# Kernel optimization log

Hardware: AMD Instinct MI355X
Metric: run time of the kernel (lower is better)

The kernel has to match this reference:

```python
import jax, jax.numpy as jnp
import numpy as np

N, C, H, W = 4, 256, 64, 64  # in_channels == out_channels == C


def conv1x1(x, w, b):
    # x: [N, Cin, H, W], w: [Cout, Cin], b: [Cout]
    return jnp.einsum('nchw,oc->nohw', x, w) + b[None, :, None, None]


def setup_inputs() -> dict:
    key = jax.random.key(0)
    ks = jax.random.split(key, 4)
    scale = 1.0 / np.sqrt(C)
    return {
        'x': jax.random.normal(ks[0], (N, C, H, W), dtype=jnp.float32),
        'theta_w': jax.random.normal(ks[1], (C, C), dtype=jnp.float32) * scale,
        'theta_b': jnp.zeros((C,), dtype=jnp.float32),
        'phi_w': jax.random.normal(ks[2], (C, C), dtype=jnp.float32) * scale,
        'phi_b': jnp.zeros((C,), dtype=jnp.float32),
        'conv1_w': jax.random.normal(ks[3], (C, C), dtype=jnp.float32) * scale,
        'conv1_b': jnp.zeros((C,), dtype=jnp.float32),
    }


def reference(x, theta_w, theta_b, phi_w, phi_b, conv1_w, conv1_b):
    n, c, h, w = x.shape
    hw = h * w
    theta = conv1x1(x, theta_w, theta_b).reshape(n, c, hw)   # queries [N,C,HW]
    phi = conv1x1(x, phi_w, phi_b).reshape(n, c, hw)         # keys    [N,C,HW]
    g = x.reshape(n, c, hw)                                   # values  [N,C,HW]
    # f = einsum('niab,nicd->nabcd') flattened: [N, HW_q, HW_k]
    scores = jnp.einsum('ncp,ncq->npq', theta, phi) / jnp.sqrt(jnp.asarray(c, x.dtype))
    attn = jax.nn.softmax(scores, axis=-1)                    # softmax over keys
    # f = einsum('nabcd,nicd->niab'): weighted sum of values
    f = jnp.einsum('npq,ncq->ncp', attn, g).reshape(n, c, h, w)
    result = conv1x1(f, conv1_w, conv1_b)
    return x + result
```

## Files before the change

kernel.cpp:

```cpp
#include <hip/hip_runtime.h>
#include <hip/hip_bf16.h>

typedef __attribute__((ext_vector_type(8))) short short8;
typedef __attribute__((ext_vector_type(4))) short short4_t;
typedef __attribute__((ext_vector_type(4))) float float4_t;
typedef unsigned short ushort;

#define HW 4096
#define CC 256
#define NBATCH 4
#define SEQ ((size_t)NBATCH * HW)

static __device__ __forceinline__ unsigned short f2b(float f) {
    union { float f; unsigned u; } v; v.f = f;
    unsigned r = v.u + 0x7FFF + ((v.u >> 16) & 1);
    return (unsigned short)(r >> 16);
}
static __device__ __forceinline__ float b2f(unsigned short u) {
    union { unsigned u; float f; } v; v.u = ((unsigned)u) << 16;
    return v.f;
}

__global__ __launch_bounds__(256) void k_prep(const float* __restrict__ x,
                                              const float* __restrict__ tw,
                                              const float* __restrict__ pw,
                                              const float* __restrict__ cw,
                                              unsigned short* __restrict__ XT,
                                              unsigned short* __restrict__ gb,
                                              unsigned short* __restrict__ Wbt,
                                              unsigned short* __restrict__ Wbp,
                                              unsigned short* __restrict__ Wbc) {
    __shared__ float T[64][65];
    int fb = blockIdx.x + 64 * (blockIdx.y + 4 * blockIdx.z);
    if (fb < 768) {
        int i = fb * 256 + threadIdx.x;
        int sel = i >> 16, off = i & 65535;
        const float* s = sel == 0 ? tw : (sel == 1 ? pw : cw);
        unsigned short* d = sel == 0 ? Wbt : (sel == 1 ? Wbp : Wbc);
        d[off] = f2b(s[off]);
    }
    int n = blockIdx.z, c0 = blockIdx.y * 64, p0 = blockIdx.x * 64;
    int t = threadIdx.x;
    int pl = t & 63, rg = t >> 6;
    const float* xp = x + ((size_t)n * CC + c0) * HW + p0;
    #pragma unroll
    for (int i = 0; i < 16; i++) {
        int cl = rg * 16 + i;
        float v = xp[(size_t)cl * HW + pl];
        T[cl][pl] = v;
        gb[((size_t)n * CC + c0 + cl) * HW + p0 + pl] = f2b(v);
    }
    __syncthreads();
    int cl = t & 63, pg = t >> 6;
    unsigned short* xt = XT + ((size_t)n * HW + p0) * CC + c0;
    #pragma unroll
    for (int i = 0; i < 16; i++) {
        int plw = pg * 16 + i;
        xt[(size_t)plw * CC + cl] = f2b(T[cl][plw]);
    }
}

__global__ __launch_bounds__(256) void k_proj(const unsigned short* __restrict__ XT,
                                              const unsigned short* __restrict__ Wt,
                                              const unsigned short* __restrict__ Wp,
                                              const float* __restrict__ bt,
                                              const float* __restrict__ bp,
                                              unsigned short* __restrict__ outT_t,
                                              unsigned short* __restrict__ outT_p) {
    const unsigned short* W; const float* b; unsigned short* outT;
    if (blockIdx.y == 0) { W = Wt; b = bt; outT = outT_t; }
    else                 { W = Wp; b = bp; outT = outT_p; }
    int w = threadIdx.x >> 6, lane = threadIdx.x & 63;
    int nidx = lane & 15, quad = lane >> 4;
    size_t row0 = (size_t)blockIdx.x * 64 + w * 16;
    float4_t acc[16];
    #pragma unroll
    for (int i = 0; i < 16; i++) acc[i] = (float4_t)(0.f);
    const unsigned short* arow = XT + (row0 + nidx) * CC + quad * 8;
    for (int ks = 0; ks < 8; ks++) {
        short8 a = *(const short8*)(arow + ks * 32);
        #pragma unroll
        for (int cb = 0; cb < 16; cb++) {
            short8 bb = *(const short8*)(W + (size_t)(cb * 16 + nidx) * CC + ks * 32 + quad * 8);
            acc[cb] = __builtin_amdgcn_mfma_f32_16x16x32_bf16(a, bb, acc[cb], 0, 0, 0);
        }
    }
    #pragma unroll
    for (int cb = 0; cb < 16; cb++) {
        int co = cb * 16 + nidx;
        float bias = b[co];
        #pragma unroll
        for (int r = 0; r < 4; r++) {
            size_t prow = row0 + quad * 4 + r;
            outT[prow * CC + co] = f2b(acc[cb][r] + bias);
        }
    }
}

__global__ __launch_bounds__(512)
void k_attn(const unsigned short* __restrict__ thetaT,
            const unsigned short* __restrict__ phiT,
            const unsigned short* __restrict__ gb,
            ushort* __restrict__ Ow, float* __restrict__ lw) {
    __shared__ __align__(16) ushort Kl[2][16384];
    __shared__ __align__(16) ushort Pbuf[2][16][64][8];
    __shared__ float Lbuf[2][128];

    const int tid = threadIdx.x;
    const int w = tid >> 6, lane = tid & 63;
    const int nidx = lane & 15, quad = lane >> 4;
    const int qg = w & 3;
    const int kh = w >> 2;
    const int nb = (blockIdx.x & 7) >> 1;
    const int h  = blockIdx.x & 1;
    const int qtile = blockIdx.x >> 3;
    const int p0 = qtile * 128;
    const size_t seq0 = (size_t)nb * HW;
    const ushort* Kg = phiT + seq0 * CC;
    const ushort* Vg = gb + (size_t)nb * CC * HW;
    const int k00 = h * 2048;

    short8 th[2][8];
    #pragma unroll
    for (int qs = 0; qs < 2; qs++) {
        const ushort* qrow = thetaT + (seq0 + p0 + qg * 32 + qs * 16 + nidx) * CC + quad * 8;
        #pragma unroll
        for (int kb = 0; kb < 8; kb++) th[qs][kb] = *(const short8*)(qrow + kb * 32);
    }

    float4_t o[2][8];
    #pragma unroll
    for (int i = 0; i < 2; i++)
        #pragma unroll
        for (int j = 0; j < 8; j++) o[i][j] = (float4_t)(0.f);
    float lrow[8];
    #pragma unroll
    for (int i = 0; i < 8; i++) lrow[i] = 0.f;

    const int c_s = tid >> 4, n_s = tid & 15;
    const int kfbase = (c_s >> 2) * 512 + ((c_s & 3) * 16 + n_s) * 8;
    auto loadKregs = [&](short8 (&kr)[4], int tt) {
        #pragma unroll
        for (int rr = 0; rr < 4; rr++)
            kr[rr] = *(const short8*)(Kg + (size_t)(k00 + tt * 64 + rr * 16 + n_s) * CC + c_s * 8);
    };
    auto stageK = [&](int buf, const short8 (&kr)[4]) {
        #pragma unroll
        for (int rr = 0; rr < 4; rr++) *(short8*)(&Kl[buf][rr * 4096 + kfbase]) = kr[rr];
    };
    auto loadVregs = [&](short8 (&vr)[4], int tt) {
        #pragma unroll
        for (int mg = 0; mg < 2; mg++)
            #pragma unroll
            for (int kst = 0; kst < 2; kst++)
                vr[mg * 2 + kst] = *(const short8*)(Vg + (size_t)(w * 32 + mg * 16 + nidx) * HW
                                                    + k00 + tt * 64 + kst * 32 + quad * 8);
    };

    const float SC = 0.0625f * 1.44269504088896f;
    const int pj = nidx & 7;
    const int pc_hi = nidx >> 3;

    float4_t s00, s01, s10, s11;
    auto expPhase = [&](int buf) {
        #pragma unroll
        for (int r = 0; r < 4; r++) {
            float e = exp2f(s00[r] * SC); lrow[r] += e;
            Pbuf[buf][(qg * 2 + 0) * 2 + kh][(0 * 2 + pc_hi) * 16 + quad * 4 + r][pj] = f2b(e);
        }
        #pragma unroll
        for (int r = 0; r < 4; r++) {
            float e = exp2f(s01[r] * SC); lrow[r] += e;
            Pbuf[buf][(qg * 2 + 0) * 2 + kh][(1 * 2 + pc_hi) * 16 + quad * 4 + r][pj] = f2b(e);
        }
        #pragma unroll
        for (int r = 0; r < 4; r++) {
            float e = exp2f(s10[r] * SC); lrow[4 + r] += e;
            Pbuf[buf][(qg * 2 + 1) * 2 + kh][(0 * 2 + pc_hi) * 16 + quad * 4 + r][pj] = f2b(e);
        }
        #pragma unroll
        for (int r = 0; r < 4; r++) {
            float e = exp2f(s11[r] * SC); lrow[4 + r] += e;
            Pbuf[buf][(qg * 2 + 1) * 2 + kh][(1 * 2 + pc_hi) * 16 + quad * 4 + r][pj] = f2b(e);
        }
    };

    short8 kregs[4], vregs[4];
    loadKregs(kregs, 0); loadVregs(vregs, 0);
    stageK(0, kregs);
    loadKregs(kregs, 1);
    __syncthreads();
    s00 = (float4_t)(0.f); s01 = (float4_t)(0.f); s10 = (float4_t)(0.f); s11 = (float4_t)(0.f);
    #pragma unroll
    for (int kb = 0; kb < 8; kb++) {
        short8 k0 = *(const short8*)(&Kl[0][((kh * 2 + 0) * 8 + kb) * 512 + lane * 8]);
        short8 k1 = *(const short8*)(&Kl[0][((kh * 2 + 1) * 8 + kb) * 512 + lane * 8]);
        s00 = __builtin_amdgcn_mfma_f32_16x16x32_bf16(th[0][kb], k0, s00, 0, 0, 0);
        s01 = __builtin_amdgcn_mfma_f32_16x16x32_bf16(th[0][kb], k1, s01, 0, 0, 0);
        s10 = __builtin_amdgcn_mfma_f32_16x16x32_bf16(th[1][kb], k0, s10, 0, 0, 0);
        s11 = __builtin_amdgcn_mfma_f32_16x16x32_bf16(th[1][kb], k1, s11, 0, 0, 0);
    }
    expPhase(0);
    stageK(1, kregs);
    loadKregs(kregs, 2);
    __syncthreads();

    #pragma unroll 1
    for (int t = 0; t < 31; t++) {
        const int pb = t & 1;
        const int kbuf = (t + 1) & 1;
        s00 = (float4_t)(0.f); s01 = (float4_t)(0.f);
        s10 = (float4_t)(0.f); s11 = (float4_t)(0.f);
        #pragma unroll
        for (int i = 0; i < 8; i++) {
            short8 k0 = *(const short8*)(&Kl[kbuf][((kh * 2 + 0) * 8 + i) * 512 + lane * 8]);
            short8 k1 = *(const short8*)(&Kl[kbuf][((kh * 2 + 1) * 8 + i) * 512 + lane * 8]);
            s00 = __builtin_amdgcn_mfma_f32_16x16x32_bf16(th[0][i], k0, s00, 0, 0, 0);
            s01 = __builtin_amdgcn_mfma_f32_16x16x32_bf16(th[0][i], k1, s01, 0, 0, 0);
            s10 = __builtin_amdgcn_mfma_f32_16x16x32_bf16(th[1][i], k0, s10, 0, 0, 0);
            s11 = __builtin_amdgcn_mfma_f32_16x16x32_bf16(th[1][i], k1, s11, 0, 0, 0);
            short8 pf0 = *(const short8*)(&Pbuf[pb][i * 2 + 0][lane][0]);
            short8 pf1 = *(const short8*)(&Pbuf[pb][i * 2 + 1][lane][0]);
            o[0][i] = __builtin_amdgcn_mfma_f32_16x16x32_bf16(vregs[0], pf0, o[0][i], 0, 0, 0);
            o[0][i] = __builtin_amdgcn_mfma_f32_16x16x32_bf16(vregs[1], pf1, o[0][i], 0, 0, 0);
            o[1][i] = __builtin_amdgcn_mfma_f32_16x16x32_bf16(vregs[2], pf0, o[1][i], 0, 0, 0);
            o[1][i] = __builtin_amdgcn_mfma_f32_16x16x32_bf16(vregs[3], pf1, o[1][i], 0, 0, 0);
        }
        loadVregs(vregs, t + 1);
        expPhase((t + 1) & 1);
        if (t < 30) {
            stageK((t + 2) & 1, kregs);
            loadKregs(kregs, (t + 3 < 32) ? t + 3 : 31);
        }
        __syncthreads();
    }
    {
        const int pb = 31 & 1;
        #pragma unroll
        for (int i = 0; i < 8; i++) {
            short8 pf0 = *(const short8*)(&Pbuf[pb][i * 2 + 0][lane][0]);
            short8 pf1 = *(const short8*)(&Pbuf[pb][i * 2 + 1][lane][0]);
            o[0][i] = __builtin_amdgcn_mfma_f32_16x16x32_bf16(vregs[0], pf0, o[0][i], 0, 0, 0);
            o[0][i] = __builtin_amdgcn_mfma_f32_16x16x32_bf16(vregs[1], pf1, o[0][i], 0, 0, 0);
            o[1][i] = __builtin_amdgcn_mfma_f32_16x16x32_bf16(vregs[2], pf0, o[1][i], 0, 0, 0);
            o[1][i] = __builtin_amdgcn_mfma_f32_16x16x32_bf16(vregs[3], pf1, o[1][i], 0, 0, 0);
        }
    }

    #pragma unroll
    for (int i = 0; i < 8; i++) {
        float v = lrow[i];
        v += __shfl_xor(v, 1);
        v += __shfl_xor(v, 2);
        v += __shfl_xor(v, 4);
        v += __shfl_xor(v, 8);
        if (nidx == 0)
            Lbuf[kh][qg * 32 + (i >> 2) * 16 + quad * 4 + (i & 3)] = v;
    }
    __syncthreads();
    if (tid < 128)
        lw[(size_t)h * SEQ + seq0 + p0 + tid] = Lbuf[0][tid] + Lbuf[1][tid];
    ushort* Op = Ow + ((size_t)h * SEQ + seq0 + p0) * CC;
    #pragma unroll
    for (int mg = 0; mg < 2; mg++)
        #pragma unroll
        for (int qq = 0; qq < 8; qq++) {
            short4_t pk;
            #pragma unroll
            for (int r = 0; r < 4; r++) pk[r] = (short)f2b(o[mg][qq][r]);
            *(short4_t*)(Op + (size_t)(qq * 16 + nidx) * CC + w * 32 + mg * 16 + quad * 4) = pk;
        }
}

__global__ __launch_bounds__(256) void k_reduce(const ushort* __restrict__ Ow,
                                                const float* __restrict__ lw,
                                                unsigned short* __restrict__ fT) {
    const short8* O0 = (const short8*)Ow;
    const short8* O1 = (const short8*)(Ow + SEQ * CC);
    int i0 = blockIdx.x * 256 + threadIdx.x;
    #pragma unroll
    for (int j = 0; j < 4; j++) {
        int idx = j * 131072 + i0;
        int row = idx >> 5;
        float li = 1.0f / (lw[row] + lw[SEQ + row]);
        short8 a = O0[idx];
        short8 b = O1[idx];
        short8 pk;
        #pragma unroll
        for (int r = 0; r < 8; r++)
            pk[r] = (short)f2b((b2f((ushort)a[r]) + b2f((ushort)b[r])) * li);
        *(short8*)(fT + (size_t)idx * 8) = pk;
    }
}

__global__ __launch_bounds__(256) void k_final(const unsigned short* __restrict__ Wc,
                                               const float* __restrict__ bc,
                                               const unsigned short* __restrict__ fT,
                                               const float* __restrict__ x,
                                               float* __restrict__ out) {
    int w = threadIdx.x >> 6, lane = threadIdx.x & 63;
    int nidx = lane & 15, quad = lane >> 4;
    int n = blockIdx.z;
    int co0 = blockIdx.y * 64 + w * 16;
    int p0 = blockIdx.x * 64;
    float4_t acc[4];
    #pragma unroll
    for (int i = 0; i < 4; i++) acc[i] = (float4_t)(0.f);
    const unsigned short* arow = Wc + (size_t)(co0 + nidx) * CC + quad * 8;
    const unsigned short* brow = fT + ((size_t)n * HW + p0 + nidx) * CC + quad * 8;
    for (int ks = 0; ks < 8; ks++) {
        short8 a = *(const short8*)(arow + ks * 32);
        #pragma unroll
        for (int pb = 0; pb < 4; pb++) {
            short8 bb = *(const short8*)(brow + (size_t)pb * 16 * CC + ks * 32);
            acc[pb] = __builtin_amdgcn_mfma_f32_16x16x32_bf16(a, bb, acc[pb], 0, 0, 0);
        }
    }
    #pragma unroll
    for (int pb = 0; pb < 4; pb++) {
        #pragma unroll
        for (int r = 0; r < 4; r++) {
            int co = co0 + quad * 4 + r;
            size_t idx = ((size_t)n * CC + co) * HW + p0 + pb * 16 + nidx;
            out[idx] = x[idx] + bc[co] + acc[pb][r];
        }
    }
}

extern "C" void kernel_launch(void* const* d_in, const int* in_sizes, int n_in,
                              void* d_out, int out_size, void* d_ws, size_t ws_size,
                              hipStream_t stream) {
    const float* x       = (const float*)d_in[0];
    const float* theta_w = (const float*)d_in[1];
    const float* theta_b = (const float*)d_in[2];
    const float* phi_w   = (const float*)d_in[3];
    const float* phi_b   = (const float*)d_in[4];
    const float* conv1_w = (const float*)d_in[5];
    const float* conv1_b = (const float*)d_in[6];
    float* out = (float*)d_out;

    unsigned short* XT  = (unsigned short*)d_ws;
    unsigned short* gb  = XT  + SEQ * CC;
    unsigned short* thT = gb  + SEQ * CC;
    unsigned short* phT = thT + SEQ * CC;
    unsigned short* fT  = phT + SEQ * CC;
    unsigned short* Wbt = fT  + SEQ * CC;
    unsigned short* Wbp = Wbt + 65536;
    unsigned short* Wbc = Wbp + 65536;
    unsigned short* Ow  = Wbc + 65536;
    float* lw = (float*)(Ow + 2 * SEQ * CC);

    k_prep<<<dim3(64, 4, 4), 256, 0, stream>>>(x, theta_w, phi_w, conv1_w, XT, gb, Wbt, Wbp, Wbc);
    k_proj<<<dim3(256, 2), 256, 0, stream>>>(XT, Wbt, Wbp, theta_b, phi_b, thT, phT);
    k_attn<<<dim3(256), 512, 0, stream>>>(thT, phT, gb, Ow, lw);
    k_reduce<<<dim3(512), 256, 0, stream>>>(Ow, lw, fT);
    k_final<<<dim3(64, 4, 4), 256, 0, stream>>>(Wbc, conv1_b, fT, x, out);
}
```

Measured before the change: 222.9 us.

## Double-buffer V registers in attention loop and fuse split-K reduce into final conv

The attention main loop is restructured into a two-way unrolled lambda that ping-pongs between two V register sets. K staging and the next K/V global loads are issued at the start of each iteration, so their latency overlaps the MFMA work. Separately, the k_reduce kernel is removed and its work (summing the two partial outputs and normalising by the softmax denominator) is done inside k_final while loading its B operand. This saves one launch and one full write and read of the intermediate. The cost is more VGPR pressure in the attention kernel, and k_final now does redundant reads of both partials for each of the 4 co-blocks.

Result: slower. 242.0 us (+8.6%).

```diff
diff --git a/kernel.cpp b/kernel.cpp
--- a/kernel.cpp
+++ b/kernel.cpp
@@ -185,30 +185,14 @@
         }
     };
 
-    short8 kregs[4], vregs[4];
-    loadKregs(kregs, 0); loadVregs(vregs, 0);
-    stageK(0, kregs);
-    loadKregs(kregs, 1);
-    __syncthreads();
-    s00 = (float4_t)(0.f); s01 = (float4_t)(0.f); s10 = (float4_t)(0.f); s11 = (float4_t)(0.f);
-    #pragma unroll
-    for (int kb = 0; kb < 8; kb++) {
-        short8 k0 = *(const short8*)(&Kl[0][((kh * 2 + 0) * 8 + kb) * 512 + lane * 8]);
-        short8 k1 = *(const short8*)(&Kl[0][((kh * 2 + 1) * 8 + kb) * 512 + lane * 8]);
-        s00 = __builtin_amdgcn_mfma_f32_16x16x32_bf16(th[0][kb], k0, s00, 0, 0, 0);
-        s01 = __builtin_amdgcn_mfma_f32_16x16x32_bf16(th[0][kb], k1, s01, 0, 0, 0);
-        s10 = __builtin_amdgcn_mfma_f32_16x16x32_bf16(th[1][kb], k0, s10, 0, 0, 0);
-        s11 = __builtin_amdgcn_mfma_f32_16x16x32_bf16(th[1][kb], k1, s11, 0, 0, 0);
-    }
-    expPhase(0);
-    stageK(1, kregs);
-    loadKregs(kregs, 2);
-    __syncthreads();
-
-    #pragma unroll 1
-    for (int t = 0; t < 31; t++) {
+    short8 kregs[4], vA[4], vB[4];
+
+    auto ITER = [&](int t, const short8 (&vCur)[4], short8 (&vNext)[4]) {
         const int pb = t & 1;
         const int kbuf = (t + 1) & 1;
+        if (t <= 29) stageK((t + 2) & 1, kregs);
+        if (t <= 28) loadKregs(kregs, t + 3);
+        loadVregs(vNext, t + 1);
         s00 = (float4_t)(0.f); s01 = (float4_t)(0.f);
         s10 = (float4_t)(0.f); s11 = (float4_t)(0.f);
         #pragma unroll
@@ -221,30 +205,48 @@
             s11 = __builtin_amdgcn_mfma_f32_16x16x32_bf16(th[1][i], k1, s11, 0, 0, 0);
             short8 pf0 = *(const short8*)(&Pbuf[pb][i * 2 + 0][lane][0]);
             short8 pf1 = *(const short8*)(&Pbuf[pb][i * 2 + 1][lane][0]);
-            o[0][i] = __builtin_amdgcn_mfma_f32_16x16x32_bf16(vregs[0], pf0, o[0][i], 0, 0, 0);
-            o[0][i] = __builtin_amdgcn_mfma_f32_16x16x32_bf16(vregs[1], pf1, o[0][i], 0, 0, 0);
-            o[1][i] = __builtin_amdgcn_mfma_f32_16x16x32_bf16(vregs[2], pf0, o[1][i], 0, 0, 0);
-            o[1][i] = __builtin_amdgcn_mfma_f32_16x16x32_bf16(vregs[3], pf1, o[1][i], 0, 0, 0);
-        }
-        loadVregs(vregs, t + 1);
+            o[0][i] = __builtin_amdgcn_mfma_f32_16x16x32_bf16(vCur[0], pf0, o[0][i], 0, 0, 0);
+            o[0][i] = __builtin_amdgcn_mfma_f32_16x16x32_bf16(vCur[1], pf1, o[0][i], 0, 0, 0);
+            o[1][i] = __builtin_amdgcn_mfma_f32_16x16x32_bf16(vCur[2], pf0, o[1][i], 0, 0, 0);
+            o[1][i] = __builtin_amdgcn_mfma_f32_16x16x32_bf16(vCur[3], pf1, o[1][i], 0, 0, 0);
+        }
         expPhase((t + 1) & 1);
-        if (t < 30) {
-            stageK((t + 2) & 1, kregs);
-            loadKregs(kregs, (t + 3 < 32) ? t + 3 : 31);
-        }
         __syncthreads();
-    }
-    {
-        const int pb = 31 & 1;
-        #pragma unroll
-        for (int i = 0; i < 8; i++) {
-            short8 pf0 = *(const short8*)(&Pbuf[pb][i * 2 + 0][lane][0]);
-            short8 pf1 = *(const short8*)(&Pbuf[pb][i * 2 + 1][lane][0]);
-            o[0][i] = __builtin_amdgcn_mfma_f32_16x16x32_bf16(vregs[0], pf0, o[0][i], 0, 0, 0);
-            o[0][i] = __builtin_amdgcn_mfma_f32_16x16x32_bf16(vregs[1], pf1, o[0][i], 0, 0, 0);
-            o[1][i] = __builtin_amdgcn_mfma_f32_16x16x32_bf16(vregs[2], pf0, o[1][i], 0, 0, 0);
-            o[1][i] = __builtin_amdgcn_mfma_f32_16x16x32_bf16(vregs[3], pf1, o[1][i], 0, 0, 0);
-        }
+    };
+
+    loadKregs(kregs, 0); loadVregs(vA, 0);
+    stageK(0, kregs);
+    loadKregs(kregs, 1);
+    __syncthreads();
+    s00 = (float4_t)(0.f); s01 = (float4_t)(0.f); s10 = (float4_t)(0.f); s11 = (float4_t)(0.f);
+    #pragma unroll
+    for (int kb = 0; kb < 8; kb++) {
+        short8 k0 = *(const short8*)(&Kl[0][((kh * 2 + 0) * 8 + kb) * 512 + lane * 8]);
+        short8 k1 = *(const short8*)(&Kl[0][((kh * 2 + 1) * 8 + kb) * 512 + lane * 8]);
+        s00 = __builtin_amdgcn_mfma_f32_16x16x32_bf16(th[0][kb], k0, s00, 0, 0, 0);
+        s01 = __builtin_amdgcn_mfma_f32_16x16x32_bf16(th[0][kb], k1, s01, 0, 0, 0);
+        s10 = __builtin_amdgcn_mfma_f32_16x16x32_bf16(th[1][kb], k0, s10, 0, 0, 0);
+        s11 = __builtin_amdgcn_mfma_f32_16x16x32_bf16(th[1][kb], k1, s11, 0, 0, 0);
+    }
+    expPhase(0);
+    stageK(1, kregs);
+    loadKregs(kregs, 2);
+    __syncthreads();
+
+    #pragma unroll 1
+    for (int tt = 0; tt < 15; tt++) {
+        ITER(tt * 2, vA, vB);
+        ITER(tt * 2 + 1, vB, vA);
+    }
+    ITER(30, vA, vB);
+    #pragma unroll
+    for (int i = 0; i < 8; i++) {
+        short8 pf0 = *(const short8*)(&Pbuf[1][i * 2 + 0][lane][0]);
+        short8 pf1 = *(const short8*)(&Pbuf[1][i * 2 + 1][lane][0]);
+        o[0][i] = __builtin_amdgcn_mfma_f32_16x16x32_bf16(vB[0], pf0, o[0][i], 0, 0, 0);
+        o[0][i] = __builtin_amdgcn_mfma_f32_16x16x32_bf16(vB[1], pf1, o[0][i], 0, 0, 0);
+        o[1][i] = __builtin_amdgcn_mfma_f32_16x16x32_bf16(vB[2], pf0, o[1][i], 0, 0, 0);
+        o[1][i] = __builtin_amdgcn_mfma_f32_16x16x32_bf16(vB[3], pf1, o[1][i], 0, 0, 0);
     }
 
     #pragma unroll
@@ -272,30 +274,10 @@
         }
 }
 
-__global__ __launch_bounds__(256) void k_reduce(const ushort* __restrict__ Ow,
-                                                const float* __restrict__ lw,
-                                                unsigned short* __restrict__ fT) {
-    const short8* O0 = (const short8*)Ow;
-    const short8* O1 = (const short8*)(Ow + SEQ * CC);
-    int i0 = blockIdx.x * 256 + threadIdx.x;
-    #pragma unroll
-    for (int j = 0; j < 4; j++) {
-        int idx = j * 131072 + i0;
-        int row = idx >> 5;
-        float li = 1.0f / (lw[row] + lw[SEQ + row]);
-        short8 a = O0[idx];
-        short8 b = O1[idx];
-        short8 pk;
-        #pragma unroll
-        for (int r = 0; r < 8; r++)
-            pk[r] = (short)f2b((b2f((ushort)a[r]) + b2f((ushort)b[r])) * li);
-        *(short8*)(fT + (size_t)idx * 8) = pk;
-    }
-}
-
 __global__ __launch_bounds__(256) void k_final(const unsigned short* __restrict__ Wc,
                                                const float* __restrict__ bc,
-                                               const unsigned short* __restrict__ fT,
+                                               const ushort* __restrict__ Ow,
+                                               const float* __restrict__ lw,
                                                const float* __restrict__ x,
                                                float* __restrict__ out) {
     int w = threadIdx.x >> 6, lane = threadIdx.x & 63;
@@ -303,16 +285,30 @@
     int n = blockIdx.z;
     int co0 = blockIdx.y * 64 + w * 16;
     int p0 = blockIdx.x * 64;
+    const ushort* O0 = Ow;
+    const ushort* O1 = Ow + SEQ * CC;
+    const size_t rowb = (size_t)n * HW + p0;
+    float li[4];
+    #pragma unroll
+    for (int pb = 0; pb < 4; pb++) {
+        size_t rg = rowb + pb * 16 + nidx;
+        li[pb] = 1.0f / (lw[rg] + lw[SEQ + rg]);
+    }
     float4_t acc[4];
     #pragma unroll
     for (int i = 0; i < 4; i++) acc[i] = (float4_t)(0.f);
     const unsigned short* arow = Wc + (size_t)(co0 + nidx) * CC + quad * 8;
-    const unsigned short* brow = fT + ((size_t)n * HW + p0 + nidx) * CC + quad * 8;
     for (int ks = 0; ks < 8; ks++) {
         short8 a = *(const short8*)(arow + ks * 32);
         #pragma unroll
         for (int pb = 0; pb < 4; pb++) {
-            short8 bb = *(const short8*)(brow + (size_t)pb * 16 * CC + ks * 32);
+            size_t off = (rowb + pb * 16 + nidx) * CC + ks * 32 + quad * 8;
+            short8 u0 = *(const short8*)(O0 + off);
+            short8 u1 = *(const short8*)(O1 + off);
+            short8 bb;
+            #pragma unroll
+            for (int r = 0; r < 8; r++)
+                bb[r] = (short)f2b((b2f((ushort)u0[r]) + b2f((ushort)u1[r])) * li[pb]);
             acc[pb] = __builtin_amdgcn_mfma_f32_16x16x32_bf16(a, bb, acc[pb], 0, 0, 0);
         }
     }
@@ -343,8 +339,7 @@
     unsigned short* gb  = XT  + SEQ * CC;
     unsigned short* thT = gb  + SEQ * CC;
     unsigned short* phT = thT + SEQ * CC;
-    unsigned short* fT  = phT + SEQ * CC;
-    unsigned short* Wbt = fT  + SEQ * CC;
+    unsigned short* Wbt = phT + SEQ * CC;
     unsigned short* Wbp = Wbt + 65536;
     unsigned short* Wbc = Wbp + 65536;
     unsigned short* Ow  = Wbc + 65536;
@@ -353,6 +348,5 @@
     k_prep<<<dim3(64, 4, 4), 256, 0, stream>>>(x, theta_w, phi_w, conv1_w, XT, gb, Wbt, Wbp, Wbc);
     k_proj<<<dim3(256, 2), 256, 0, stream>>>(XT, Wbt, Wbp, theta_b, phi_b, thT, phT);
     k_attn<<<dim3(256), 512, 0, stream>>>(thT, phT, gb, Ow, lw);
-    k_reduce<<<dim3(512), 256, 0, stream>>>(Ow, lw, fT);
-    k_final<<<dim3(64, 4, 4), 256, 0, stream>>>(Wbc, conv1_b, fT, x, out);
-}
+    k_final<<<dim3(64, 4, 4), 256, 0, stream>>>(Wbc, conv1_b, Ow, lw, x, out);
+}
```

## Transpose score MFMAs, vectorize swizzled P stores, double-buffer V registers

Applied to the files above, without the earlier changes.

The score MFMAs now take K as the A operand and theta as B, so each lane holds four consecutive keys for one query. This lets the exponentiated probabilities be packed into one 4-element store per tile, with an XOR swizzle on the Pbuf row index to reduce LDS bank conflicts. The row-sum accumulators shrink from 8 to 2 and are reduced across quads instead of within rows. The main loop is unrolled by two with ping-pong V register sets, so the next V load does not overwrite registers still being consumed. The cost is higher register pressure, and the swizzled read and write indices must match exactly.

After: 213.4 us. 4.3% less time.

```diff
diff --git a/kernel.cpp b/kernel.cpp
--- a/kernel.cpp
+++ b/kernel.cpp
@@ -133,9 +133,7 @@
     for (int i = 0; i < 2; i++)
         #pragma unroll
         for (int j = 0; j < 8; j++) o[i][j] = (float4_t)(0.f);
-    float lrow[8];
-    #pragma unroll
-    for (int i = 0; i < 8; i++) lrow[i] = 0.f;
+    float lrow[2] = {0.f, 0.f};
 
     const int c_s = tid >> 4, n_s = tid & 15;
     const int kfbase = (c_s >> 2) * 512 + ((c_s & 3) * 16 + n_s) * 8;
@@ -158,35 +156,68 @@
     };
 
     const float SC = 0.0625f * 1.44269504088896f;
-    const int pj = nidx & 7;
-    const int pc_hi = nidx >> 3;
+    const int Gp = quad >> 1;
+    const int pcell_lo = (nidx ^ (Gp * 4));
+    const int pj0 = (quad & 1) * 4;
+    const int prcell = ((lane >> 4) << 4) | ((lane & 15) ^ (((lane >> 4) & 1) * 4));
 
     float4_t s00, s01, s10, s11;
     auto expPhase = [&](int buf) {
-        #pragma unroll
-        for (int r = 0; r < 4; r++) {
-            float e = exp2f(s00[r] * SC); lrow[r] += e;
-            Pbuf[buf][(qg * 2 + 0) * 2 + kh][(0 * 2 + pc_hi) * 16 + quad * 4 + r][pj] = f2b(e);
-        }
-        #pragma unroll
-        for (int r = 0; r < 4; r++) {
-            float e = exp2f(s01[r] * SC); lrow[r] += e;
-            Pbuf[buf][(qg * 2 + 0) * 2 + kh][(1 * 2 + pc_hi) * 16 + quad * 4 + r][pj] = f2b(e);
-        }
-        #pragma unroll
-        for (int r = 0; r < 4; r++) {
-            float e = exp2f(s10[r] * SC); lrow[4 + r] += e;
-            Pbuf[buf][(qg * 2 + 1) * 2 + kh][(0 * 2 + pc_hi) * 16 + quad * 4 + r][pj] = f2b(e);
-        }
-        #pragma unroll
-        for (int r = 0; r < 4; r++) {
-            float e = exp2f(s11[r] * SC); lrow[4 + r] += e;
-            Pbuf[buf][(qg * 2 + 1) * 2 + kh][(1 * 2 + pc_hi) * 16 + quad * 4 + r][pj] = f2b(e);
-        }
-    };
-
-    short8 kregs[4], vregs[4];
-    loadKregs(kregs, 0); loadVregs(vregs, 0);
+        short4_t pk;
+        #pragma unroll
+        for (int r = 0; r < 4; r++) {
+            float e = exp2f(s00[r] * SC); lrow[0] += e; pk[r] = (short)f2b(e);
+        }
+        *(short4_t*)(&Pbuf[buf][(qg * 2 + 0) * 2 + kh][(0 * 2 + Gp) * 16 + pcell_lo][pj0]) = pk;
+        #pragma unroll
+        for (int r = 0; r < 4; r++) {
+            float e = exp2f(s01[r] * SC); lrow[1] += e; pk[r] = (short)f2b(e);
+        }
+        *(short4_t*)(&Pbuf[buf][(qg * 2 + 1) * 2 + kh][(0 * 2 + Gp) * 16 + pcell_lo][pj0]) = pk;
+        #pragma unroll
+        for (int r = 0; r < 4; r++) {
+            float e = exp2f(s10[r] * SC); lrow[0] += e; pk[r] = (short)f2b(e);
+        }
+        *(short4_t*)(&Pbuf[buf][(qg * 2 + 0) * 2 + kh][(1 * 2 + Gp) * 16 + pcell_lo][pj0]) = pk;
+        #pragma unroll
+        for (int r = 0; r < 4; r++) {
+            float e = exp2f(s11[r] * SC); lrow[1] += e; pk[r] = (short)f2b(e);
+        }
+        *(short4_t*)(&Pbuf[buf][(qg * 2 + 1) * 2 + kh][(1 * 2 + Gp) * 16 + pcell_lo][pj0]) = pk;
+    };
+
+    short8 kregs[4], vA[4], vB[4];
+
+    auto ITER = [&](int t, const short8 (&vCur)[4], short8 (&vNext)[4]) {
+        const int pb = t & 1;
+        const int kbuf = (t + 1) & 1;
+        s00 = (float4_t)(0.f); s01 = (float4_t)(0.f);
+        s10 = (float4_t)(0.f); s11 = (float4_t)(0.f);
+        #pragma unroll
+        for (int i = 0; i < 8; i++) {
+            short8 k0 = *(const short8*)(&Kl[kbuf][((kh * 2 + 0) * 8 + i) * 512 + lane * 8]);
+            short8 k1 = *(const short8*)(&Kl[kbuf][((kh * 2 + 1) * 8 + i) * 512 + lane * 8]);
+            s00 = __builtin_amdgcn_mfma_f32_16x16x32_bf16(k0, th[0][i], s00, 0, 0, 0);
+            s01 = __builtin_amdgcn_mfma_f32_16x16x32_bf16(k0, th[1][i], s01, 0, 0, 0);
+            s10 = __builtin_amdgcn_mfma_f32_16x16x32_bf16(k1, th[0][i], s10, 0, 0, 0);
+            s11 = __builtin_amdgcn_mfma_f32_16x16x32_bf16(k1, th[1][i], s11, 0, 0, 0);
+            short8 pf0 = *(const short8*)(&Pbuf[pb][i * 2 + 0][prcell][0]);
+            short8 pf1 = *(const short8*)(&Pbuf[pb][i * 2 + 1][prcell][0]);
+            o[0][i] = __builtin_amdgcn_mfma_f32_16x16x32_bf16(vCur[0], pf0, o[0][i], 0, 0, 0);
+            o[0][i] = __builtin_amdgcn_mfma_f32_16x16x32_bf16(vCur[1], pf1, o[0][i], 0, 0, 0);
+            o[1][i] = __builtin_amdgcn_mfma_f32_16x16x32_bf16(vCur[2], pf0, o[1][i], 0, 0, 0);
+            o[1][i] = __builtin_amdgcn_mfma_f32_16x16x32_bf16(vCur[3], pf1, o[1][i], 0, 0, 0);
+        }
+        loadVregs(vNext, t + 1);
+        expPhase((t + 1) & 1);
+        if (t < 30) {
+            stageK((t + 2) & 1, kregs);
+            loadKregs(kregs, (t + 3 < 32) ? t + 3 : 31);
+        }
+        __syncthreads();
+    };
+
+    loadKregs(kregs, 0); loadVregs(vA, 0);
     stageK(0, kregs);
     loadKregs(kregs, 1);
     __syncthreads();
@@ -195,10 +226,10 @@
     for (int kb = 0; kb < 8; kb++) {
         short8 k0 = *(const short8*)(&Kl[0][((kh * 2 + 0) * 8 + kb) * 512 + lane * 8]);
         short8 k1 = *(const short8*)(&Kl[0][((kh * 2 + 1) * 8 + kb) * 512 + lane * 8]);
-        s00 = __builtin_amdgcn_mfma_f32_16x16x32_bf16(th[0][kb], k0, s00, 0, 0, 0);
-        s01 = __builtin_amdgcn_mfma_f32_16x16x32_bf16(th[0][kb], k1, s01, 0, 0, 0);
-        s10 = __builtin_amdgcn_mfma_f32_16x16x32_bf16(th[1][kb], k0, s10, 0, 0, 0);
-        s11 = __builtin_amdgcn_mfma_f32_16x16x32_bf16(th[1][kb], k1, s11, 0, 0, 0);
+        s00 = __builtin_amdgcn_mfma_f32_16x16x32_bf16(k0, th[0][kb], s00, 0, 0, 0);
+        s01 = __builtin_amdgcn_mfma_f32_16x16x32_bf16(k0, th[1][kb], s01, 0, 0, 0);
+        s10 = __builtin_amdgcn_mfma_f32_16x16x32_bf16(k1, th[0][kb], s10, 0, 0, 0);
+        s11 = __builtin_amdgcn_mfma_f32_16x16x32_bf16(k1, th[1][kb], s11, 0, 0, 0);
     }
     expPhase(0);
     stageK(1, kregs);
@@ -206,56 +237,27 @@
     __syncthreads();
 
     #pragma unroll 1
-    for (int t = 0; t < 31; t++) {
-        const int pb = t & 1;
-        const int kbuf = (t + 1) & 1;
-        s00 = (float4_t)(0.f); s01 = (float4_t)(0.f);
-        s10 = (float4_t)(0.f); s11 = (float4_t)(0.f);
-        #pragma unroll
-        for (int i = 0; i < 8; i++) {
-            short8 k0 = *(const short8*)(&Kl[kbuf][((kh * 2 + 0) * 8 + i) * 512 + lane * 8]);
-            short8 k1 = *(const short8*)(&Kl[kbuf][((kh * 2 + 1) * 8 + i) * 512 + lane * 8]);
-            s00 = __builtin_amdgcn_mfma_f32_16x16x32_bf16(th[0][i], k0, s00, 0, 0, 0);
-            s01 = __builtin_amdgcn_mfma_f32_16x16x32_bf16(th[0][i], k1, s01, 0, 0, 0);
-            s10 = __builtin_amdgcn_mfma_f32_16x16x32_bf16(th[1][i], k0, s10, 0, 0, 0);
-            s11 = __builtin_amdgcn_mfma_f32_16x16x32_bf16(th[1][i], k1, s11, 0, 0, 0);
-            short8 pf0 = *(const short8*)(&Pbuf[pb][i * 2 + 0][lane][0]);
-            short8 pf1 = *(const short8*)(&Pbuf[pb][i * 2 + 1][lane][0]);
-            o[0][i] = __builtin_amdgcn_mfma_f32_16x16x32_bf16(vregs[0], pf0, o[0][i], 0, 0, 0);
-            o[0][i] = __builtin_amdgcn_mfma_f32_16x16x32_bf16(vregs[1], pf1, o[0][i], 0, 0, 0);
-            o[1][i] = __builtin_amdgcn_mfma_f32_16x16x32_bf16(vregs[2], pf0, o[1][i], 0, 0, 0);
-            o[1][i] = __builtin_amdgcn_mfma_f32_16x16x32_bf16(vregs[3], pf1, o[1][i], 0, 0, 0);
-        }
-        loadVregs(vregs, t + 1);
-        expPhase((t + 1) & 1);
-        if (t < 30) {
-            stageK((t + 2) & 1, kregs);
-            loadKregs(kregs, (t + 3 < 32) ? t + 3 : 31);
-        }
-        __syncthreads();
-    }
-    {
-        const int pb = 31 & 1;
-        #pragma unroll
-        for (int i = 0; i < 8; i++) {
-            short8 pf0 = *(const short8*)(&Pbuf[pb][i * 2 + 0][lane][0]);
-            short8 pf1 = *(const short8*)(&Pbuf[pb][i * 2 + 1][lane][0]);
-            o[0][i] = __builtin_amdgcn_mfma_f32_16x16x32_bf16(vregs[0], pf0, o[0][i], 0, 0, 0);
-            o[0][i] = __builtin_amdgcn_mfma_f32_16x16x32_bf16(vregs[1], pf1, o[0][i], 0, 0, 0);
-            o[1][i] = __builtin_amdgcn_mfma_f32_16x16x32_bf16(vregs[2], pf0, o[1][i], 0, 0, 0);
-            o[1][i] = __builtin_amdgcn_mfma_f32_16x16x32_bf16(vregs[3], pf1, o[1][i], 0, 0, 0);
-        }
-    }
-
+    for (int tt = 0; tt < 15; tt++) {
+        ITER(tt * 2, vA, vB);
+        ITER(tt * 2 + 1, vB, vA);
+    }
+    ITER(30, vA, vB);
     #pragma unroll
     for (int i = 0; i < 8; i++) {
-        float v = lrow[i];
-        v += __shfl_xor(v, 1);
-        v += __shfl_xor(v, 2);
-        v += __shfl_xor(v, 4);
-        v += __shfl_xor(v, 8);
-        if (nidx == 0)
-            Lbuf[kh][qg * 32 + (i >> 2) * 16 + quad * 4 + (i & 3)] = v;
+        short8 pf0 = *(const short8*)(&Pbuf[1][i * 2 + 0][prcell][0]);
+        short8 pf1 = *(const short8*)(&Pbuf[1][i * 2 + 1][prcell][0]);
+        o[0][i] = __builtin_amdgcn_mfma_f32_16x16x32_bf16(vB[0], pf0, o[0][i], 0, 0, 0);
+        o[0][i] = __builtin_amdgcn_mfma_f32_16x16x32_bf16(vB[1], pf1, o[0][i], 0, 0, 0);
+        o[1][i] = __builtin_amdgcn_mfma_f32_16x16x32_bf16(vB[2], pf0, o[1][i], 0, 0, 0);
+        o[1][i] = __builtin_amdgcn_mfma_f32_16x16x32_bf16(vB[3], pf1, o[1][i], 0, 0, 0);
+    }
+
+    #pragma unroll
+    for (int qs = 0; qs < 2; qs++) {
+        float v = lrow[qs];
+        v += __shfl_xor(v, 16);
+        v += __shfl_xor(v, 32);
+        if (quad == 0) Lbuf[kh][qg * 32 + qs * 16 + nidx] = v;
     }
     __syncthreads();
     if (tid < 128)
```
